# Optimization experiments

Measured on AMD Instinct MI355X. Metric: run time of the kernel, lower is better.

## Reference

```python
import jax, jax.numpy as jnp
import numpy as np

B, T, F, H = 2048, 512, 64, 16


def setup_inputs() -> dict:
    key = jax.random.key(0)
    ks = jax.random.split(key, 10)
    s = 0.05  # small init so relu-activated LSTM state stays bounded over 512 steps
    return {
        "x": jax.random.normal(ks[0], (B, T, F), dtype=jnp.float32),
        "Wx": jax.random.normal(ks[1], (F, 4 * H), dtype=jnp.float32) * s,
        "Wh": jax.random.normal(ks[2], (H, 4 * H), dtype=jnp.float32) * s,
        "b": jnp.zeros((4 * H,), dtype=jnp.float32),
        "W2": jax.random.normal(ks[3], (H, 8), dtype=jnp.float32) * 0.3,
        "b2": jnp.zeros((8,), dtype=jnp.float32),
        "W3": jax.random.normal(ks[4], (8, 4), dtype=jnp.float32) * 0.3,
        "b3": jnp.zeros((4,), dtype=jnp.float32),
        "Wo": jax.random.normal(ks[5], (4, 1), dtype=jnp.float32) * 0.3,
        "bo": jnp.zeros((1,), dtype=jnp.float32),
    }


def reference(x, Wx, Wh, b, W2, b2, W3, b3, Wo, bo):
    # Keras LSTM, gate order [i, f, c(g), o]; recurrent_activation=sigmoid,
    # activation=relu (applied to candidate g AND to cell state in h = o*relu(c)).
    # Precompute input projections for all timesteps, scan only the recurrence.
    xz = jnp.einsum('btf,fg->btg', x, Wx) + b  # [B, T, 4H]
    h0 = jnp.zeros((x.shape[0], H), dtype=x.dtype)
    c0 = jnp.zeros((x.shape[0], H), dtype=x.dtype)

    def step(carry, xz_t):
        h, c = carry
        z = xz_t + h @ Wh  # [B, 4H]
        i = jax.nn.sigmoid(z[:, 0 * H:1 * H])
        f = jax.nn.sigmoid(z[:, 1 * H:2 * H])
        g = jax.nn.relu(z[:, 2 * H:3 * H])
        o = jax.nn.sigmoid(z[:, 3 * H:4 * H])
        c_new = f * c + i * g
        h_new = o * jax.nn.relu(c_new)
        return (h_new, c_new), None

    (h_T, _), _ = jax.lax.scan(step, (h0, c0), jnp.swapaxes(xz, 0, 1))
    # Dropout layers are identity at inference (training=False).
    x2 = jax.nn.relu(h_T @ W2 + b2)
    x3 = jax.nn.relu(x2 @ W3 + b3)
    return jax.nn.sigmoid(x3 @ Wo + bo)  # [B, 1]
```

## Files before the change

### kernel.cpp

```cpp
#include <hip/hip_runtime.h>
#include <stdint.h>

#define Bdim 2048
#define Tdim 512
#define NBLK (Tdim / 16)

#define TSTRIDE 68
#define BUFD (16 * TSTRIDE)

typedef __attribute__((ext_vector_type(8))) short bf16x8;
typedef __attribute__((ext_vector_type(4))) float f32x4;

__device__ __forceinline__ uint16_t f2bf(float f) {
    union { float f; uint32_t u; } v; v.f = f;
    uint32_t r = v.u + 0x7fffu + ((v.u >> 16) & 1u);
    return (uint16_t)(r >> 16);
}
__device__ __forceinline__ float sigmoidf(float z) {
    return __builtin_amdgcn_rcpf(1.0f + __expf(-z));
}

__global__ __launch_bounds__(64, 2) void lstm_fused(
    const float* __restrict__ x, const float* __restrict__ Wx,
    const float* __restrict__ bias, const float* __restrict__ Wh,
    const float* __restrict__ W2, const float* __restrict__ b2,
    const float* __restrict__ W3, const float* __restrict__ b3,
    const float* __restrict__ Wo, const float* __restrict__ bo,
    float* __restrict__ out)
{
    __shared__ __align__(16) float zbuf[2 * BUFD];
    __shared__ __align__(16) float hbuf[16];

    const int lane = threadIdx.x;
    const int l15  = lane & 15;
    const int quad = lane >> 4;
    const int b    = blockIdx.x;

    float w[16];
    #pragma unroll
    for (int k = 0; k < 16; ++k) w[k] = Wh[(size_t)k * 64 + lane];

    bf16x8 wxf[4][2];
    #pragma unroll
    for (int nt = 0; nt < 4; ++nt)
        #pragma unroll
        for (int kc = 0; kc < 2; ++kc)
            #pragma unroll
            for (int jj = 0; jj < 8; ++jj)
                wxf[nt][kc][jj] =
                    (short)f2bf(Wx[(size_t)(kc * 32 + quad * 8 + jj) * 64 + nt * 16 + l15]);

    float bv[4];
    #pragma unroll
    for (int nt = 0; nt < 4; ++nt) bv[nt] = bias[nt * 16 + l15];

    float4 xn[4];
    auto load_tile = [&](int t0) {
        const float* p = x + ((size_t)b * Tdim + t0 + l15) * 64 + quad * 8;
        xn[0] = *(const float4*)(p);
        xn[1] = *(const float4*)(p + 4);
        xn[2] = *(const float4*)(p + 32);
        xn[3] = *(const float4*)(p + 36);
    };

    auto project = [&](int q) {
        bf16x8 af[2];
        #pragma unroll
        for (int kc = 0; kc < 2; ++kc) {
            const float4 p0 = xn[kc * 2], p1 = xn[kc * 2 + 1];
            af[kc][0] = (short)f2bf(p0.x); af[kc][1] = (short)f2bf(p0.y);
            af[kc][2] = (short)f2bf(p0.z); af[kc][3] = (short)f2bf(p0.w);
            af[kc][4] = (short)f2bf(p1.x); af[kc][5] = (short)f2bf(p1.y);
            af[kc][6] = (short)f2bf(p1.z); af[kc][7] = (short)f2bf(p1.w);
        }
        f32x4 acc[4];
        #pragma unroll
        for (int nt = 0; nt < 4; ++nt) {
            f32x4 a = {bv[nt], bv[nt], bv[nt], bv[nt]};
            a = __builtin_amdgcn_mfma_f32_16x16x32_bf16(af[0], wxf[nt][0], a, 0, 0, 0);
            a = __builtin_amdgcn_mfma_f32_16x16x32_bf16(af[1], wxf[nt][1], a, 0, 0, 0);
            acc[nt] = a;
        }
        #pragma unroll
        for (int reg = 0; reg < 4; ++reg) {
            float4 w4;
            w4.x = acc[0][reg]; w4.y = acc[1][reg];
            w4.z = acc[2][reg]; w4.w = acc[3][reg];
            *(float4*)&zbuf[q * BUFD + (quad * 4 + reg) * TSTRIDE + l15 * 4] = w4;
        }
    };

    const int zoff = l15 * 4 + quad;
    auto readz = [&](int q, int t) -> float {
        return zbuf[q * BUFD + t * TSTRIDE + zoff];
    };

    load_tile(0);
    project(0);
    load_tile(16);

    float c = 0.f, h = 0.f;
    float hk[16];
    #pragma unroll
    for (int k = 0; k < 16; ++k) hk[k] = 0.f;
    float zc = readz(0, 0);

    for (int n = 0; n < NBLK; ++n) {
        const int p = n & 1;
        if (n + 1 < NBLK) {
            project(p ^ 1);
            if (n + 2 < NBLK) load_tile((n + 2) * 16);
        }
        #pragma unroll
        for (int u = 0; u < 16; ++u) {
            float zn = (u < 15) ? readz(p, u + 1) : readz(p ^ 1, 0);

            float a0 = zc, a1 = 0.f;
            #pragma unroll
            for (int k = 0; k < 8; ++k) {
                a0 = fmaf(hk[k],     w[k],     a0);
                a1 = fmaf(hk[k + 8], w[k + 8], a1);
            }
            const float z = a0 + a1;
            const float sig = sigmoidf(z);
            const float a = (quad == 2) ? fmaxf(z, 0.f) : sig;

            const float i_ = __shfl(a, l15);
            const float f_ = __shfl(a, l15 + 16);
            const float g_ = __shfl(a, l15 + 32);
            const float o_ = __shfl(a, l15 + 48);

            c = fmaf(f_, c, i_ * g_);
            h = o_ * fmaxf(c, 0.f);

            hbuf[l15] = h;
            const float4* hb = (const float4*)hbuf;
            float4 h0 = hb[0], h1 = hb[1], h2 = hb[2], h3 = hb[3];
            hk[0]  = h0.x; hk[1]  = h0.y; hk[2]  = h0.z; hk[3]  = h0.w;
            hk[4]  = h1.x; hk[5]  = h1.y; hk[6]  = h1.z; hk[7]  = h1.w;
            hk[8]  = h2.x; hk[9]  = h2.y; hk[10] = h2.z; hk[11] = h2.w;
            hk[12] = h3.x; hk[13] = h3.y; hk[14] = h3.z; hk[15] = h3.w;

            zc = zn;
        }
    }

    if (lane == 0) {
        float x2[8];
        #pragma unroll
        for (int k = 0; k < 8; ++k) {
            float s = b2[k];
            #pragma unroll
            for (int q = 0; q < 16; ++q) s = fmaf(hk[q], W2[(size_t)q * 8 + k], s);
            x2[k] = fmaxf(s, 0.f);
        }
        float x3[4];
        #pragma unroll
        for (int m = 0; m < 4; ++m) {
            float s = b3[m];
            #pragma unroll
            for (int k = 0; k < 8; ++k) s = fmaf(x2[k], W3[(size_t)k * 4 + m], s);
            x3[m] = fmaxf(s, 0.f);
        }
        float s = bo[0];
        #pragma unroll
        for (int m = 0; m < 4; ++m) s = fmaf(x3[m], Wo[m], s);
        out[b] = sigmoidf(s);
    }
}

extern "C" void kernel_launch(void* const* d_in, const int* in_sizes, int n_in,
                              void* d_out, int out_size, void* d_ws, size_t ws_size,
                              hipStream_t stream) {
    const float* x  = (const float*)d_in[0];
    const float* Wx = (const float*)d_in[1];
    const float* Wh = (const float*)d_in[2];
    const float* bb = (const float*)d_in[3];
    const float* W2 = (const float*)d_in[4];
    const float* b2 = (const float*)d_in[5];
    const float* W3 = (const float*)d_in[6];
    const float* b3 = (const float*)d_in[7];
    const float* Wo = (const float*)d_in[8];
    const float* bo = (const float*)d_in[9];

    lstm_fused<<<Bdim, 64, 0, stream>>>(x, Wx, bb, Wh, W2, b2, W3, b3,
                                        Wo, bo, (float*)d_out);
}
```

Baseline: 386.0 us.

## Broadcast hidden state via DPP row rotates instead of LDS round-trip

Replaces the per-step LDS write/read of the hidden vector with 15 DPP row-rotate operations, using Wh loaded in a rotated order so each lane's dot product works on rotated h. Gate exchange switches to xor-shuffles with selects. The sigmoid scale -log2(e) is folded into the weights and bias so a raw exp2 can be used. The z-buffer layout is changed to allow float4 reads every four steps, with double-buffered x prefetch. The intent is to shorten the serial per-step latency of the recurrence, at the cost of more intricate lane-index bookkeeping.

```diff
diff --git a/kernel.cpp b/kernel.cpp
--- a/kernel.cpp
+++ b/kernel.cpp
@@ -3,13 +3,12 @@
 
 #define Bdim 2048
 #define Tdim 512
-#define NBLK (Tdim / 16)
-
-#define TSTRIDE 68
-#define BUFD (16 * TSTRIDE)
+#define NTILE 32
 
 typedef __attribute__((ext_vector_type(8))) short bf16x8;
 typedef __attribute__((ext_vector_type(4))) float f32x4;
+
+union U32x4 { uint32_t u[4]; bf16x8 v; };
 
 __device__ __forceinline__ uint16_t f2bf(float f) {
     union { float f; uint32_t u; } v; v.f = f;
@@ -19,6 +18,19 @@
 __device__ __forceinline__ float sigmoidf(float z) {
     return __builtin_amdgcn_rcpf(1.0f + __expf(-z));
 }
+__device__ __forceinline__ float fast_exp2(float x) {
+#if __has_builtin(__builtin_amdgcn_exp2f)
+    return __builtin_amdgcn_exp2f(x);
+#else
+    return exp2f(x);
+#endif
+}
+
+#define RORF(M, dst, src)                                                     \
+    dst = __int_as_float(__builtin_amdgcn_update_dpp(                         \
+        __float_as_int(src), __float_as_int(src), 0x120 | (M), 0xF, 0xF, 0))
+#define RORI(M, dst, src)                                                     \
+    dst = __builtin_amdgcn_update_dpp((src), (src), 0x120 | (M), 0xF, 0xF, 0)
 
 __global__ __launch_bounds__(64, 2) void lstm_fused(
     const float* __restrict__ x, const float* __restrict__ Wx,
@@ -28,130 +40,146 @@
     const float* __restrict__ Wo, const float* __restrict__ bo,
     float* __restrict__ out)
 {
-    __shared__ __align__(16) float zbuf[2 * BUFD];
-    __shared__ __align__(16) float hbuf[16];
+    __shared__ __align__(16) float zbuf[2048];
+    __shared__ float hs[16];
 
     const int lane = threadIdx.x;
-    const int l15  = lane & 15;
+    const int u    = lane & 15;
     const int quad = lane >> 4;
+    const int col  = quad * 16 + u;
     const int b    = blockIdx.x;
+    const float NL2E = -1.4426950408889634f;
+    const float sg   = (quad == 2) ? 1.0f : NL2E;
 
     float w[16];
+    w[0] = Wh[(size_t)u * 64 + col] * sg;
+#define WL(M) { int ii_; RORI(M, ii_, u); w[M] = Wh[(size_t)ii_ * 64 + col] * sg; }
+    WL(1)  WL(2)  WL(3)  WL(4)  WL(5)  WL(6)  WL(7)
+    WL(8)  WL(9)  WL(10) WL(11) WL(12) WL(13) WL(14) WL(15)
+#undef WL
+
+    bf16x8 wxf[4][2];
+    float bv[4];
     #pragma unroll
-    for (int k = 0; k < 16; ++k) w[k] = Wh[(size_t)k * 64 + lane];
-
-    bf16x8 wxf[4][2];
-    #pragma unroll
-    for (int nt = 0; nt < 4; ++nt)
+    for (int nt = 0; nt < 4; ++nt) {
+        const float s = (nt == 2) ? 1.0f : NL2E;
         #pragma unroll
         for (int kc = 0; kc < 2; ++kc)
             #pragma unroll
-            for (int jj = 0; jj < 8; ++jj)
-                wxf[nt][kc][jj] =
-                    (short)f2bf(Wx[(size_t)(kc * 32 + quad * 8 + jj) * 64 + nt * 16 + l15]);
-
-    float bv[4];
-    #pragma unroll
-    for (int nt = 0; nt < 4; ++nt) bv[nt] = bias[nt * 16 + l15];
-
-    float4 xn[4];
-    auto load_tile = [&](int t0) {
-        const float* p = x + ((size_t)b * Tdim + t0 + l15) * 64 + quad * 8;
-        xn[0] = *(const float4*)(p);
-        xn[1] = *(const float4*)(p + 4);
-        xn[2] = *(const float4*)(p + 32);
-        xn[3] = *(const float4*)(p + 36);
+            for (int e = 0; e < 8; ++e)
+                wxf[nt][kc][e] = (short)f2bf(
+                    Wx[(size_t)(kc * 32 + quad * 8 + e) * 64 + nt * 16 + u] * s);
+        bv[nt] = bias[nt * 16 + u] * s;
+    }
+
+    f32x4 xa0[4], xa1[4];
+    auto xload = [&](int tile, f32x4 (&xs)[4]) {
+        const float* p = x + ((size_t)b * Tdim + tile * 16 + u) * 64 + quad * 8;
+        xs[0] = *(const f32x4*)(p);
+        xs[1] = *(const f32x4*)(p + 4);
+        xs[2] = *(const f32x4*)(p + 32);
+        xs[3] = *(const f32x4*)(p + 36);
     };
 
-    auto project = [&](int q) {
-        bf16x8 af[2];
+    auto proj = [&](const f32x4 (&xs)[4], int buf) {
+        U32x4 af[2];
         #pragma unroll
         for (int kc = 0; kc < 2; ++kc) {
-            const float4 p0 = xn[kc * 2], p1 = xn[kc * 2 + 1];
-            af[kc][0] = (short)f2bf(p0.x); af[kc][1] = (short)f2bf(p0.y);
-            af[kc][2] = (short)f2bf(p0.z); af[kc][3] = (short)f2bf(p0.w);
-            af[kc][4] = (short)f2bf(p1.x); af[kc][5] = (short)f2bf(p1.y);
-            af[kc][6] = (short)f2bf(p1.z); af[kc][7] = (short)f2bf(p1.w);
-        }
-        f32x4 acc[4];
+            asm("v_cvt_pk_bf16_f32 %0, %1, %2" : "=v"(af[kc].u[0]) : "v"(xs[2*kc][0]),   "v"(xs[2*kc][1]));
+            asm("v_cvt_pk_bf16_f32 %0, %1, %2" : "=v"(af[kc].u[1]) : "v"(xs[2*kc][2]),   "v"(xs[2*kc][3]));
+            asm("v_cvt_pk_bf16_f32 %0, %1, %2" : "=v"(af[kc].u[2]) : "v"(xs[2*kc+1][0]), "v"(xs[2*kc+1][1]));
+            asm("v_cvt_pk_bf16_f32 %0, %1, %2" : "=v"(af[kc].u[3]) : "v"(xs[2*kc+1][2]), "v"(xs[2*kc+1][3]));
+        }
+        float* zb = zbuf + buf * 1024 + quad * 256 + u * 4;
         #pragma unroll
         for (int nt = 0; nt < 4; ++nt) {
             f32x4 a = {bv[nt], bv[nt], bv[nt], bv[nt]};
-            a = __builtin_amdgcn_mfma_f32_16x16x32_bf16(af[0], wxf[nt][0], a, 0, 0, 0);
-            a = __builtin_amdgcn_mfma_f32_16x16x32_bf16(af[1], wxf[nt][1], a, 0, 0, 0);
-            acc[nt] = a;
-        }
-        #pragma unroll
-        for (int reg = 0; reg < 4; ++reg) {
-            float4 w4;
-            w4.x = acc[0][reg]; w4.y = acc[1][reg];
-            w4.z = acc[2][reg]; w4.w = acc[3][reg];
-            *(float4*)&zbuf[q * BUFD + (quad * 4 + reg) * TSTRIDE + l15 * 4] = w4;
+            a = __builtin_amdgcn_mfma_f32_16x16x32_bf16(af[0].v, wxf[nt][0], a, 0, 0, 0);
+            a = __builtin_amdgcn_mfma_f32_16x16x32_bf16(af[1].v, wxf[nt][1], a, 0, 0, 0);
+            *(f32x4*)(zb + nt * 64) = a;
         }
     };
 
-    const int zoff = l15 * 4 + quad;
-    auto readz = [&](int q, int t) -> float {
-        return zbuf[q * BUFD + t * TSTRIDE + zoff];
+    xload(0, xa0);
+    proj(xa0, 0);
+    xload(1, xa1);
+
+    float c = 0.f, h = 0.f;
+    f32x4 zgA = *(const f32x4*)(zbuf + col * 4);
+    f32x4 zgB;
+
+    const bool q0 = (lane & 16) != 0;
+    const bool q1 = (lane & 32) != 0;
+    const bool isrelu = (quad == 2);
+
+    auto scan_tile = [&](int n) {
+        #pragma unroll
+        for (int t = 0; t < 16; ++t) {
+            const int gl = t >> 2;
+            if ((t & 3) == 0) {
+                const int gg = n * 4 + gl + 1;
+                if (gg < 4 * NTILE) {
+                    const float* zp = zbuf + ((gg >> 2) & 1) * 1024
+                                    + (gg & 3) * 256 + col * 4;
+                    f32x4 zv = *(const f32x4*)zp;
+                    if (gl & 1) zgA = zv; else zgB = zv;
+                }
+            }
+            const float zval = (gl & 1) ? zgB[t & 3] : zgA[t & 3];
+
+            float acc0 = fmaf(h, w[0], zval), acc1 = 0.f, hr;
+#define DOT(M, A_) { RORF(M, hr, h); A_ = fmaf(hr, w[M], A_); }
+            DOT(1,  acc1) DOT(2,  acc0) DOT(3,  acc1) DOT(4,  acc0)
+            DOT(5,  acc1) DOT(6,  acc0) DOT(7,  acc1) DOT(8,  acc0)
+            DOT(9,  acc1) DOT(10, acc0) DOT(11, acc1) DOT(12, acc0)
+            DOT(13, acc1) DOT(14, acc0) DOT(15, acc1)
+#undef DOT
+            const float zacc = acc0 + acc1;
+
+            const float sig = __builtin_amdgcn_rcpf(1.0f + fast_exp2(zacc));
+            const float a   = isrelu ? fmaxf(zacc, 0.0f) : sig;
+
+            const float a16 = __shfl_xor(a, 16, 64);
+            const float a32 = __shfl_xor(a, 32, 64);
+            const float a48 = __shfl_xor(a16, 32, 64);
+            const float A1 = q0 ? a16 : a;
+            const float B1 = q0 ? a48 : a32;
+            const float A2 = q0 ? a   : a16;
+            const float B2 = q0 ? a32 : a48;
+            const float gi = q1 ? B1 : A1;
+            const float gG = q1 ? A1 : B1;
+            const float gf = q1 ? B2 : A2;
+            const float go = q1 ? A2 : B2;
+
+            c = fmaf(gf, c, gi * gG);
+            h = go * fmaxf(c, 0.0f);
+        }
     };
 
-    load_tile(0);
-    project(0);
-    load_tile(16);
-
-    float c = 0.f, h = 0.f;
-    float hk[16];
-    #pragma unroll
-    for (int k = 0; k < 16; ++k) hk[k] = 0.f;
-    float zc = readz(0, 0);
-
-    for (int n = 0; n < NBLK; ++n) {
-        const int p = n & 1;
-        if (n + 1 < NBLK) {
-            project(p ^ 1);
-            if (n + 2 < NBLK) load_tile((n + 2) * 16);
-        }
-        #pragma unroll
-        for (int u = 0; u < 16; ++u) {
-            float zn = (u < 15) ? readz(p, u + 1) : readz(p ^ 1, 0);
-
-            float a0 = zc, a1 = 0.f;
-            #pragma unroll
-            for (int k = 0; k < 8; ++k) {
-                a0 = fmaf(hk[k],     w[k],     a0);
-                a1 = fmaf(hk[k + 8], w[k + 8], a1);
-            }
-            const float z = a0 + a1;
-            const float sig = sigmoidf(z);
-            const float a = (quad == 2) ? fmaxf(z, 0.f) : sig;
-
-            const float i_ = __shfl(a, l15);
-            const float f_ = __shfl(a, l15 + 16);
-            const float g_ = __shfl(a, l15 + 32);
-            const float o_ = __shfl(a, l15 + 48);
-
-            c = fmaf(f_, c, i_ * g_);
-            h = o_ * fmaxf(c, 0.f);
-
-            hbuf[l15] = h;
-            const float4* hb = (const float4*)hbuf;
-            float4 h0 = hb[0], h1 = hb[1], h2 = hb[2], h3 = hb[3];
-            hk[0]  = h0.x; hk[1]  = h0.y; hk[2]  = h0.z; hk[3]  = h0.w;
-            hk[4]  = h1.x; hk[5]  = h1.y; hk[6]  = h1.z; hk[7]  = h1.w;
-            hk[8]  = h2.x; hk[9]  = h2.y; hk[10] = h2.z; hk[11] = h2.w;
-            hk[12] = h3.x; hk[13] = h3.y; hk[14] = h3.z; hk[15] = h3.w;
-
-            zc = zn;
+    #pragma unroll 1
+    for (int nn = 0; nn < NTILE / 2; ++nn) {
+        {
+            const int n = 2 * nn;
+            if (n + 2 < NTILE) xload(n + 2, xa0);
+            proj(xa1, 1);
+            scan_tile(n);
+        }
+        {
+            const int n = 2 * nn + 1;
+            if (n + 2 < NTILE) xload(n + 2, xa1);
+            if (n + 1 < NTILE) proj(xa0, 0);
+            scan_tile(n);
         }
     }
 
+    if (lane < 16) hs[lane] = h;
     if (lane == 0) {
         float x2[8];
         #pragma unroll
         for (int k = 0; k < 8; ++k) {
             float s = b2[k];
             #pragma unroll
-            for (int q = 0; q < 16; ++q) s = fmaf(hk[q], W2[(size_t)q * 8 + k], s);
+            for (int q = 0; q < 16; ++q) s = fmaf(hs[q], W2[(size_t)q * 8 + k], s);
             x2[k] = fmaxf(s, 0.f);
         }
         float x3[4];
```

After: 425.0 us. 1.1x slower.
